# Optimization experiments

Hardware: AMD Instinct MI355X
Metric: run time of the kernel (lower is better)

## Reference

```python
import jax, jax.numpy as jnp
import numpy as np

N_NODES = 100000
N_EDGES = 1600000
NFEAT = 128
NHID = 128
NCLASS = 40


def gcn_conv(x, W, b, src, dst, n_nodes):
    """PyG-style GCNConv: x' = D^{-1/2}(A+I)D^{-1/2} (x W) + b."""
    h = x @ W  # [N, out]
    loop = jnp.arange(n_nodes, dtype=src.dtype)
    s = jnp.concatenate([src, loop])  # add self-loops
    d = jnp.concatenate([dst, loop])
    deg = jax.ops.segment_sum(jnp.ones_like(s, dtype=h.dtype), d, num_segments=n_nodes)
    dinv = jnp.where(deg > 0, jax.lax.rsqrt(deg), 0.0)
    norm = dinv[s] * dinv[d]  # [E+N]
    msg = h[s] * norm[:, None]  # gather + scale
    out = jax.ops.segment_sum(msg, d, num_segments=n_nodes)  # scatter-add
    return out + b


def setup_inputs() -> dict:
    key = jax.random.key(0)
    ks = jax.random.split(key, 6)
    x = jax.random.normal(ks[0], (N_NODES, NFEAT), dtype=jnp.float32)
    edge_index = jax.random.randint(ks[1], (2, N_EDGES), 0, N_NODES, dtype=jnp.int64)
    sc1 = 1.0 / np.sqrt(NFEAT)
    sc2 = 1.0 / np.sqrt(NHID)
    W1 = jax.random.normal(ks[2], (NFEAT, NHID), dtype=jnp.float32) * sc1
    b1 = jnp.zeros((NHID,), dtype=jnp.float32)
    Wm = jax.random.normal(ks[3], (NHID, NHID), dtype=jnp.float32) * sc2
    bm = jnp.zeros((NHID,), dtype=jnp.float32)
    W2 = jax.random.normal(ks[4], (NHID, NCLASS), dtype=jnp.float32) * sc2
    b2 = jnp.zeros((NCLASS,), dtype=jnp.float32)
    return {"x": x, "edge_index": edge_index, "W1": W1, "b1": b1,
            "Wm": Wm, "bm": bm, "W2": W2, "b2": b2}


def reference(x, edge_index, W1, b1, Wm, bm, W2, b2):
    # StandGCNX forward, eval mode (dropout = identity)
    src, dst = edge_index[0], edge_index[1]
    n = x.shape[0]
    h = jax.nn.relu(gcn_conv(x, W1, b1, src, dst, n))
    h = jax.nn.relu(gcn_conv(h, Wm, bm, src, dst, n))
    out = gcn_conv(h, W2, b2, src, dst, n)
    return out
```

## Files before the change

kernel.cpp:

```cpp
#include <hip/hip_runtime.h>
#include <hip/hip_bf16.h>

typedef __attribute__((ext_vector_type(8))) short bf16x8;
typedef __attribute__((ext_vector_type(4))) float f32x4;

__device__ __forceinline__ ushort bf16rne(float f) {
    uint u = __float_as_uint(f);
    return (ushort)((u + 0x7fffu + ((u >> 16) & 1u)) >> 16);
}
__device__ __forceinline__ void unpack2(uint p, float& a, float& b) {
    a = __uint_as_float(p << 16);
    b = __uint_as_float(p & 0xffff0000u);
}


__global__ __launch_bounds__(256) void k_pre1(const float* __restrict__ W1,
                                              const float* __restrict__ Wm,
                                              const float* __restrict__ W2,
                                              ushort* __restrict__ w1t,
                                              ushort* __restrict__ wmt,
                                              ushort* __restrict__ w2t,
                                              const int* __restrict__ dst,
                                              int* __restrict__ bcnt, int E) {
    __shared__ int hist[512];
    int b = blockIdx.x;
    int t = threadIdx.x;
    if (b < 152) {
        if (b < 64) {
            int i = b * 256 + t; int k = i >> 7, n = i & 127;
            w1t[n * 128 + k] = bf16rne(W1[k * 128 + n]);
        } else if (b < 128) {
            int i = (b - 64) * 256 + t; int k = i >> 7, n = i & 127;
            wmt[n * 128 + k] = bf16rne(Wm[k * 128 + n]);
        } else {
            int i = (b - 128) * 256 + t;
            if (i < 6144) {
                int n = i >> 7, k = i & 127;
                w2t[n * 128 + k] = (n < 40) ? bf16rne(W2[k * 40 + n]) : (ushort)0;
            }
        }
        return;
    }
    hist[t] = 0; hist[t + 256] = 0;
    __syncthreads();
    int off = (b - 152) * 4096;
    int cnt = min(4096, E - off);
    for (int i = t; i < cnt; i += 256) atomicAdd(&hist[dst[off + i] >> 8], 1);
    __syncthreads();
    if (hist[t]) atomicAdd(&bcnt[t], hist[t]);
    if (hist[t + 256]) atomicAdd(&bcnt[t + 256], hist[t + 256]);
}

__global__ void k_bscan(const int* __restrict__ bcnt, int* __restrict__ bbase,
                        int* __restrict__ bcur, int nbuck) {
    __shared__ int s[512];
    int t = threadIdx.x;
    s[t] = (t < nbuck) ? bcnt[t] : 0;
    __syncthreads();
    for (int d = 1; d < 512; d <<= 1) {
        int u = (t >= d) ? s[t - d] : 0;
        __syncthreads();
        if (t >= d) s[t] += u;
        __syncthreads();
    }
    int excl = (t == 0) ? 0 : s[t - 1];
    bbase[t] = excl;
    if (t < nbuck) bcur[t] = excl;
    if (t == 511) bbase[512] = s[511];
}

__global__ __launch_bounds__(256) void k_binpack(const int* __restrict__ src,
                                                 const int* __restrict__ dst,
                                                 int* __restrict__ bcur,
                                                 uint* __restrict__ pairbuf,
                                                 int E, int nbuck) {
    __shared__ int hist[512];
    __shared__ int scn[512];
    __shared__ int cur[512];
    __shared__ int gbase[512];
    __shared__ uint sorted[4096];
    int t = threadIdx.x;
    int off = blockIdx.x * 4096;
    int cnt = min(4096, E - off);

    hist[t] = 0; hist[t + 256] = 0;
    __syncthreads();
    for (int i = t; i < cnt; i += 256) {
        int b = dst[off + i] >> 8;
        atomicAdd(&hist[b], 1);
    }
    __syncthreads();
    scn[t] = hist[t]; scn[t + 256] = hist[t + 256];
    __syncthreads();
    for (int d = 1; d < 256; d <<= 1) {
        int u0 = (t >= d) ? scn[t - d] : 0;
        int u1 = (t >= d) ? scn[256 + t - d] : 0;
        __syncthreads();
        if (t >= d) { scn[t] += u0; scn[256 + t] += u1; }
        __syncthreads();
    }
    int tot0 = scn[255];
    scn[256 + t] += tot0;
    __syncthreads();
    cur[t] = (t == 0) ? 0 : scn[t - 1];
    cur[t + 256] = scn[t + 255];
    if (t < nbuck && hist[t] > 0) gbase[t] = atomicAdd(&bcur[t], hist[t]);
    int t2 = t + 256;
    if (t2 < nbuck && hist[t2] > 0) gbase[t2] = atomicAdd(&bcur[t2], hist[t2]);
    __syncthreads();
    for (int i = t; i < cnt; i += 256) {
        int d = dst[off + i];
        int s = src[off + i];
        int b = d >> 8;
        int pos = atomicAdd(&cur[b], 1);
        sorted[pos] = ((uint)(d & 255) << 24) | (uint)s;
    }
    __syncthreads();
    int wid = t >> 6, lane = t & 63;
    for (int b = wid; b < nbuck; b += 4) {
        int n = hist[b];
        if (n == 0) continue;
        int ls = (b == 0) ? 0 : scn[b - 1];
        int gb = gbase[b];
        for (int j = lane; j < n; j += 64)
            pairbuf[gb + j] = sorted[ls + j];
    }
}


#define CSR_CAP 5632
__global__ __launch_bounds__(256) void k_mega(const uint* __restrict__ pairbuf,
                                              const int* __restrict__ bbase,
                                              int* __restrict__ rowptr,
                                              float* __restrict__ dinv,
                                              int* __restrict__ csr,
                                              int N, int nbuck,
                                              const float* __restrict__ A,
                                              const ushort* __restrict__ Wt,
                                              ushort* __restrict__ C, int M) {
    __shared__ int lhist[256];
    __shared__ int scn[256];
    __shared__ int lcur[256];
    __shared__ int lcsr[CSR_CAP];
    int t = threadIdx.x;
    if ((int)blockIdx.x >= nbuck) {
        int blk = blockIdx.x - nbuck;
        int wave = t >> 6, lane = t & 63;
        int m16 = lane & 15, quad = lane >> 4;
        int rowA = blk * 64 + wave * 16 + m16;
        int rA = min(rowA, M - 1);
        const float4* A4 = (const float4*)A;

        f32x4 acc[8];
#pragma unroll
        for (int i = 0; i < 8; i++) acc[i] = (f32x4){0.f, 0.f, 0.f, 0.f};
#pragma unroll
        for (int it = 0; it < 4; it++) {
            float4 f0 = A4[(size_t)rA * 32 + 8 * it + 2 * quad];
            float4 f1 = A4[(size_t)rA * 32 + 8 * it + 2 * quad + 1];
            bf16x8 af;
            af[0] = (short)bf16rne(f0.x); af[1] = (short)bf16rne(f0.y);
            af[2] = (short)bf16rne(f0.z); af[3] = (short)bf16rne(f0.w);
            af[4] = (short)bf16rne(f1.x); af[5] = (short)bf16rne(f1.y);
            af[6] = (short)bf16rne(f1.z); af[7] = (short)bf16rne(f1.w);
#pragma unroll
            for (int nt = 0; nt < 8; nt++) {
                bf16x8 bfr = *(const bf16x8*)(Wt + (size_t)(nt * 16 + m16) * 128 + it * 32 + quad * 8);
                acc[nt] = __builtin_amdgcn_mfma_f32_16x16x32_bf16(af, bfr, acc[nt], 0, 0, 0);
            }
        }
        int rowBase = blk * 64 + wave * 16 + quad * 4;
#pragma unroll
        for (int nt = 0; nt < 8; nt++) {
            int col = nt * 16 + m16;
#pragma unroll
            for (int r = 0; r < 4; r++) {
                int row = rowBase + r;
                if (row < M) C[(size_t)row * 128 + col] = bf16rne(acc[nt][r]);
            }
        }
        return;
    }
    int b = blockIdx.x;
    int base = b << 8;
    int nn = min(256, N - base);
    int lo = bbase[b], hi = bbase[b + 1];
    int cnt = hi - lo;
    lhist[t] = 0;
    __syncthreads();
    for (int i = t; i < cnt; i += 256) atomicAdd(&lhist[pairbuf[lo + i] >> 24], 1);
    __syncthreads();
    int mydeg = lhist[t];
    scn[t] = mydeg;
    __syncthreads();
    for (int d = 1; d < 256; d <<= 1) {
        int u = (t >= d) ? scn[t - d] : 0;
        __syncthreads();
        if (t >= d) scn[t] += u;
        __syncthreads();
    }
    int excl = (t == 0) ? 0 : scn[t - 1];
    lcur[t] = excl;
    if (t < nn) {
        rowptr[base + t] = lo + excl;
        dinv[base + t] = rsqrtf((float)(mydeg + 1));
    }
    if (b == nbuck - 1 && t == 0) rowptr[N] = hi;
    __syncthreads();
    if (cnt <= CSR_CAP) {
        for (int i = t; i < cnt; i += 256) {
            uint p = pairbuf[lo + i];
            int pos = atomicAdd(&lcur[p >> 24], 1);
            lcsr[pos] = (int)(p & 0xFFFFFFu);
        }
        __syncthreads();
        for (int i = t; i < cnt; i += 256) csr[lo + i] = lcsr[i];
    } else {
        for (int i = t; i < cnt; i += 256) {
            uint p = pairbuf[lo + i];
            int pos = lo + atomicAdd(&lcur[p >> 24], 1);
            csr[pos] = (int)(p & 0xFFFFFFu);
        }
    }
}


template <int NT>
__device__ __forceinline__ void fused_agg_gemm(const ushort* __restrict__ g,
                                               const float* __restrict__ dinv,
                                               const int* __restrict__ rowptr,
                                               const int* __restrict__ csr,
                                               const float* __restrict__ bias,
                                               const ushort* __restrict__ Wt,
                                               ushort* __restrict__ C,
                                               int M, int ccols) {
    __shared__ ushort hs[32][136];
    __shared__ int nextNode;
    int t = threadIdx.x;
    if (t == 0) nextNode = 0;
    int l = t & 15;
    const uint4* g16 = (const uint4*)g;
    float4 bb0 = ((const float4*)bias)[2 * l];
    float4 bb1 = ((const float4*)bias)[2 * l + 1];
    __syncthreads();

    for (;;) {
        int idx = 0;
        if (l == 0) idx = atomicAdd(&nextNode, 1);
        idx = __shfl(idx, (t & 63) & ~15, 64);
        if (idx >= 32) break;
        int node = blockIdx.x * 32 + idx;
        int nd = min(node, M - 1);
        float dn = dinv[nd];
        float a[8];
        {
            uint4 p = g16[(size_t)nd * 16 + l];
            float u, v;
            unpack2(p.x, u, v); a[0] = u * dn; a[1] = v * dn;
            unpack2(p.y, u, v); a[2] = u * dn; a[3] = v * dn;
            unpack2(p.z, u, v); a[4] = u * dn; a[5] = v * dn;
            unpack2(p.w, u, v); a[6] = u * dn; a[7] = v * dn;
        }
        int e0 = rowptr[nd], e1 = rowptr[nd + 1];
        int e = e0;
        for (; e + 4 <= e1; e += 4) {
            int s0 = csr[e], s1 = csr[e + 1], s2 = csr[e + 2], s3 = csr[e + 3];
            float w0 = dinv[s0], w1 = dinv[s1], w2 = dinv[s2], w3 = dinv[s3];
            uint4 p0 = g16[(size_t)s0 * 16 + l];
            uint4 p1 = g16[(size_t)s1 * 16 + l];
            uint4 p2 = g16[(size_t)s2 * 16 + l];
            uint4 p3 = g16[(size_t)s3 * 16 + l];
            float u, v;
            unpack2(p0.x, u, v); a[0] += u * w0; a[1] += v * w0;
            unpack2(p0.y, u, v); a[2] += u * w0; a[3] += v * w0;
            unpack2(p0.z, u, v); a[4] += u * w0; a[5] += v * w0;
            unpack2(p0.w, u, v); a[6] += u * w0; a[7] += v * w0;
            unpack2(p1.x, u, v); a[0] += u * w1; a[1] += v * w1;
            unpack2(p1.y, u, v); a[2] += u * w1; a[3] += v * w1;
            unpack2(p1.z, u, v); a[4] += u * w1; a[5] += v * w1;
            unpack2(p1.w, u, v); a[6] += u * w1; a[7] += v * w1;
            unpack2(p2.x, u, v); a[0] += u * w2; a[1] += v * w2;
            unpack2(p2.y, u, v); a[2] += u * w2; a[3] += v * w2;
            unpack2(p2.z, u, v); a[4] += u * w2; a[5] += v * w2;
            unpack2(p2.w, u, v); a[6] += u * w2; a[7] += v * w2;
            unpack2(p3.x, u, v); a[0] += u * w3; a[1] += v * w3;
            unpack2(p3.y, u, v); a[2] += u * w3; a[3] += v * w3;
            unpack2(p3.z, u, v); a[4] += u * w3; a[5] += v * w3;
            unpack2(p3.w, u, v); a[6] += u * w3; a[7] += v * w3;
        }
        for (; e < e1; e++) {
            int s = csr[e];
            float w = dinv[s];
            uint4 p = g16[(size_t)s * 16 + l];
            float u, v;
            unpack2(p.x, u, v); a[0] += u * w; a[1] += v * w;
            unpack2(p.y, u, v); a[2] += u * w; a[3] += v * w;
            unpack2(p.z, u, v); a[4] += u * w; a[5] += v * w;
            unpack2(p.w, u, v); a[6] += u * w; a[7] += v * w;
        }
        float o0 = fmaxf(a[0] * dn + bb0.x, 0.f);
        float o1 = fmaxf(a[1] * dn + bb0.y, 0.f);
        float o2 = fmaxf(a[2] * dn + bb0.z, 0.f);
        float o3 = fmaxf(a[3] * dn + bb0.w, 0.f);
        float o4 = fmaxf(a[4] * dn + bb1.x, 0.f);
        float o5 = fmaxf(a[5] * dn + bb1.y, 0.f);
        float o6 = fmaxf(a[6] * dn + bb1.z, 0.f);
        float o7 = fmaxf(a[7] * dn + bb1.w, 0.f);
        uint4 qv;
        qv.x = (uint)bf16rne(o0) | ((uint)bf16rne(o1) << 16);
        qv.y = (uint)bf16rne(o2) | ((uint)bf16rne(o3) << 16);
        qv.z = (uint)bf16rne(o4) | ((uint)bf16rne(o5) << 16);
        qv.w = (uint)bf16rne(o6) | ((uint)bf16rne(o7) << 16);
        *(uint4*)&hs[idx][l * 8] = qv;
    }
    __syncthreads();

    int wave = t >> 6, lane = t & 63;
    int m16 = lane & 15, quad = lane >> 4;
    int rowHalf = wave & 1;
    int ntHalf = wave >> 1;
    constexpr int NTH = (NT + 1) / 2;
    int ntStart = ntHalf * NTH;
    int ntEnd = ntHalf ? NT : NTH;

    f32x4 acc[NTH];
#pragma unroll
    for (int i = 0; i < NTH; i++) acc[i] = (f32x4){0.f, 0.f, 0.f, 0.f};
#pragma unroll
    for (int it = 0; it < 4; it++) {
        bf16x8 af = *(const bf16x8*)&hs[rowHalf * 16 + m16][it * 32 + quad * 8];
        for (int nt = ntStart; nt < ntEnd; nt++) {
            bf16x8 bfr = *(const bf16x8*)(Wt + (size_t)(nt * 16 + m16) * 128 + it * 32 + quad * 8);
            acc[nt - ntStart] = __builtin_amdgcn_mfma_f32_16x16x32_bf16(af, bfr, acc[nt - ntStart], 0, 0, 0);
        }
    }
    int rowBase = blockIdx.x * 32 + rowHalf * 16 + quad * 4;
    for (int nt = ntStart; nt < ntEnd; nt++) {
        int col = nt * 16 + m16;
        if (col >= ccols) continue;
#pragma unroll
        for (int r = 0; r < 4; r++) {
            int row = rowBase + r;
            if (row < M) C[(size_t)row * ccols + col] = bf16rne(acc[nt - ntStart][r]);
        }
    }
}

__global__ __launch_bounds__(256) void k_fusedA(const ushort* __restrict__ g,
                                                const float* __restrict__ dinv,
                                                const int* __restrict__ rowptr,
                                                const int* __restrict__ csr,
                                                const float* __restrict__ bias,
                                                const ushort* __restrict__ Wt,
                                                ushort* __restrict__ C, int M) {
    fused_agg_gemm<8>(g, dinv, rowptr, csr, bias, Wt, C, M, 128);
}

__global__ __launch_bounds__(256) void k_fusedB(const ushort* __restrict__ g,
                                                const float* __restrict__ dinv,
                                                const int* __restrict__ rowptr,
                                                const int* __restrict__ csr,
                                                const float* __restrict__ bias,
                                                const ushort* __restrict__ Wt,
                                                ushort* __restrict__ C, int M) {
    fused_agg_gemm<3>(g, dinv, rowptr, csr, bias, Wt, C, M, 40);
}


__global__ __launch_bounds__(256) void k_agg40_b(const ushort* __restrict__ g3,
                                                 const float* __restrict__ dinv,
                                                 const int* __restrict__ rowptr,
                                                 const int* __restrict__ csr,
                                                 const float* __restrict__ bias,
                                                 float* __restrict__ out, int N) {
    int t = threadIdx.x;
    if (t >= 250) return;
    int grp = t / 10;
    int l = t - grp * 10;
    int node = blockIdx.x * 25 + grp;
    if (node >= N) return;
    const uint2* gp = (const uint2*)g3;
    float dn = dinv[node];
    float a0, a1, a2, a3;
    {
        uint2 p = gp[(size_t)node * 10 + l];
        float u, v;
        unpack2(p.x, u, v); a0 = u * dn; a1 = v * dn;
        unpack2(p.y, u, v); a2 = u * dn; a3 = v * dn;
    }
    int e0 = rowptr[node], e1 = rowptr[node + 1];
    int e = e0;
    for (; e + 4 <= e1; e += 4) {
        int s0 = csr[e], s1 = csr[e + 1], s2 = csr[e + 2], s3 = csr[e + 3];
        float w0 = dinv[s0], w1 = dinv[s1], w2 = dinv[s2], w3 = dinv[s3];
        uint2 p0 = gp[(size_t)s0 * 10 + l];
        uint2 p1 = gp[(size_t)s1 * 10 + l];
        uint2 p2 = gp[(size_t)s2 * 10 + l];
        uint2 p3 = gp[(size_t)s3 * 10 + l];
        float u, v;
        unpack2(p0.x, u, v); a0 += u * w0; a1 += v * w0;
        unpack2(p0.y, u, v); a2 += u * w0; a3 += v * w0;
        unpack2(p1.x, u, v); a0 += u * w1; a1 += v * w1;
        unpack2(p1.y, u, v); a2 += u * w1; a3 += v * w1;
        unpack2(p2.x, u, v); a0 += u * w2; a1 += v * w2;
        unpack2(p2.y, u, v); a2 += u * w2; a3 += v * w2;
        unpack2(p3.x, u, v); a0 += u * w3; a1 += v * w3;
        unpack2(p3.y, u, v); a2 += u * w3; a3 += v * w3;
    }
    for (; e < e1; e++) {
        int s = csr[e];
        float w = dinv[s];
        uint2 p = gp[(size_t)s * 10 + l];
        float u, v;
        unpack2(p.x, u, v); a0 += u * w; a1 += v * w;
        unpack2(p.y, u, v); a2 += u * w; a3 += v * w;
    }
    float4 bb = ((const float4*)bias)[l];
    float4 o;
    o.x = a0 * dn + bb.x;
    o.y = a1 * dn + bb.y;
    o.z = a2 * dn + bb.z;
    o.w = a3 * dn + bb.w;
    ((float4*)out)[(size_t)node * 10 + l] = o;
}


extern "C" void kernel_launch(void* const* d_in, const int* in_sizes, int n_in,
                              void* d_out, int out_size, void* d_ws, size_t ws_size,
                              hipStream_t stream) {
    const float* x  = (const float*)d_in[0];
    const int* eidx = (const int*)d_in[1];
    const float* W1 = (const float*)d_in[2];
    const float* b1 = (const float*)d_in[3];
    const float* Wm = (const float*)d_in[4];
    const float* bm = (const float*)d_in[5];
    const float* W2 = (const float*)d_in[6];
    const float* b2 = (const float*)d_in[7];
    float* out = (float*)d_out;

    int N = in_sizes[0] / 128;
    int E = in_sizes[1] / 2;
    const int* src = eidx;
    const int* dst = eidx + E;
    int nbuck = (N + 255) >> 8;
    int ntile = (E + 4095) / 4096;

    char* ws = (char*)d_ws;
    size_t off = 0;
    auto alloc = [&](size_t bytes) -> void* {
        void* p = ws + off;
        off += (bytes + 255) & ~(size_t)255;
        return p;
    };
    float*  dinv    = (float*)alloc((size_t)N * 4);
    int*    rowptr  = (int*)alloc(((size_t)N + 1) * 4);
    int*    csr     = (int*)alloc((size_t)E * 4);
    uint*   pairbuf = (uint*)alloc((size_t)E * 4);
    int*    bcnt    = (int*)alloc(512 * 4);
    int*    bbase   = (int*)alloc(513 * 4);
    int*    bcur    = (int*)alloc(512 * 4);
    ushort* w1t     = (ushort*)alloc(128 * 128 * 2);
    ushort* wmt     = (ushort*)alloc(128 * 128 * 2);
    ushort* w2t     = (ushort*)alloc(48 * 128 * 2);
    ushort* gbuf    = (ushort*)alloc((size_t)N * 128 * 2);
    ushort* gbuf2   = (ushort*)alloc((size_t)N * 128 * 2);
    ushort* g3      = (ushort*)alloc((size_t)N * 40 * 2);

    int gblk64 = (N + 63) / 64;
    int gblk32 = (N + 31) / 32;

    hipMemsetAsync(bcnt, 0, 512 * 4, stream);
    k_pre1<<<152 + ntile, 256, 0, stream>>>(W1, Wm, W2, w1t, wmt, w2t, dst, bcnt, E);
    k_bscan<<<1, 512, 0, stream>>>(bcnt, bbase, bcur, nbuck);
    k_binpack<<<ntile, 256, 0, stream>>>(src, dst, bcur, pairbuf, E, nbuck);
    k_mega<<<nbuck + gblk64, 256, 0, stream>>>(pairbuf, bbase, rowptr, dinv, csr,
                                               N, nbuck, x, w1t, gbuf, N);
    k_fusedA<<<gblk32, 256, 0, stream>>>(gbuf, dinv, rowptr, csr, b1, wmt, gbuf2, N);
    k_fusedB<<<gblk32, 256, 0, stream>>>(gbuf2, dinv, rowptr, csr, bm, w2t, g3, N);
    k_agg40_b<<<(N + 24) / 25, 256, 0, stream>>>(g3, dinv, rowptr, csr, b2, out, N);
}
```

Baseline: 391.0 us.

## Fold source-side dinv scaling into GEMM epilogue and move x@W1 into binpack kernel

The fused aggregation+GEMM kernels now multiply each output row by dinv before storing, so the next layer's neighbour aggregation can sum pre-scaled rows without a per-edge dinv gather and multiply. Layer 1 still gathers dinv per edge, while layers 2 and 3 drop those random loads. Separately, the first x@W1 GEMM now runs alongside the binpack kernel instead of the CSR-build kernel, and CSR build becomes its own launch. This cuts random per-edge memory traffic in two aggregations, at the cost of reshuffling which work runs concurrently.

```diff
diff --git a/kernel.cpp b/kernel.cpp
--- a/kernel.cpp
+++ b/kernel.cpp
@@ -69,20 +69,61 @@
     if (t == 511) bbase[512] = s[511];
 }
 
-__global__ __launch_bounds__(256) void k_binpack(const int* __restrict__ src,
-                                                 const int* __restrict__ dst,
-                                                 int* __restrict__ bcur,
-                                                 uint* __restrict__ pairbuf,
-                                                 int E, int nbuck) {
+
+__global__ __launch_bounds__(256) void k_pack_gemm(const int* __restrict__ src,
+                                                   const int* __restrict__ dst,
+                                                   int* __restrict__ bcur,
+                                                   uint* __restrict__ pairbuf,
+                                                   int E, int nbuck, int ntile,
+                                                   const float* __restrict__ A,
+                                                   const ushort* __restrict__ Wt,
+                                                   ushort* __restrict__ C, int M) {
     __shared__ int hist[512];
     __shared__ int scn[512];
     __shared__ int cur[512];
     __shared__ int gbase[512];
     __shared__ uint sorted[4096];
     int t = threadIdx.x;
+    if ((int)blockIdx.x >= ntile) {
+        int blk = blockIdx.x - ntile;
+        int wave = t >> 6, lane = t & 63;
+        int m16 = lane & 15, quad = lane >> 4;
+        int rowA = blk * 64 + wave * 16 + m16;
+        int rA = min(rowA, M - 1);
+        const float4* A4 = (const float4*)A;
+
+        f32x4 acc[8];
+#pragma unroll
+        for (int i = 0; i < 8; i++) acc[i] = (f32x4){0.f, 0.f, 0.f, 0.f};
+#pragma unroll
+        for (int it = 0; it < 4; it++) {
+            float4 f0 = A4[(size_t)rA * 32 + 8 * it + 2 * quad];
+            float4 f1 = A4[(size_t)rA * 32 + 8 * it + 2 * quad + 1];
+            bf16x8 af;
+            af[0] = (short)bf16rne(f0.x); af[1] = (short)bf16rne(f0.y);
+            af[2] = (short)bf16rne(f0.z); af[3] = (short)bf16rne(f0.w);
+            af[4] = (short)bf16rne(f1.x); af[5] = (short)bf16rne(f1.y);
+            af[6] = (short)bf16rne(f1.z); af[7] = (short)bf16rne(f1.w);
+#pragma unroll
+            for (int nt = 0; nt < 8; nt++) {
+                bf16x8 bfr = *(const bf16x8*)(Wt + (size_t)(nt * 16 + m16) * 128 + it * 32 + quad * 8);
+                acc[nt] = __builtin_amdgcn_mfma_f32_16x16x32_bf16(af, bfr, acc[nt], 0, 0, 0);
+            }
+        }
+        int rowBase = blk * 64 + wave * 16 + quad * 4;
+#pragma unroll
+        for (int nt = 0; nt < 8; nt++) {
+            int col = nt * 16 + m16;
+#pragma unroll
+            for (int r = 0; r < 4; r++) {
+                int row = rowBase + r;
+                if (row < M) C[(size_t)row * 128 + col] = bf16rne(acc[nt][r]);
+            }
+        }
+        return;
+    }
     int off = blockIdx.x * 4096;
     int cnt = min(4096, E - off);
-
     hist[t] = 0; hist[t + 256] = 0;
     __syncthreads();
     for (int i = t; i < cnt; i += 256) {
@@ -127,65 +168,23 @@
     }
 }
 
-
 #define CSR_CAP 5632
-__global__ __launch_bounds__(256) void k_mega(const uint* __restrict__ pairbuf,
-                                              const int* __restrict__ bbase,
-                                              int* __restrict__ rowptr,
-                                              float* __restrict__ dinv,
-                                              int* __restrict__ csr,
-                                              int N, int nbuck,
-                                              const float* __restrict__ A,
-                                              const ushort* __restrict__ Wt,
-                                              ushort* __restrict__ C, int M) {
+__global__ __launch_bounds__(256) void k_csrbuild(const uint* __restrict__ pairbuf,
+                                                  const int* __restrict__ bbase,
+                                                  int* __restrict__ rowptr,
+                                                  float* __restrict__ dinv,
+                                                  int* __restrict__ csr,
+                                                  int N, int nbuck) {
     __shared__ int lhist[256];
     __shared__ int scn[256];
     __shared__ int lcur[256];
     __shared__ int lcsr[CSR_CAP];
-    int t = threadIdx.x;
-    if ((int)blockIdx.x >= nbuck) {
-        int blk = blockIdx.x - nbuck;
-        int wave = t >> 6, lane = t & 63;
-        int m16 = lane & 15, quad = lane >> 4;
-        int rowA = blk * 64 + wave * 16 + m16;
-        int rA = min(rowA, M - 1);
-        const float4* A4 = (const float4*)A;
-
-        f32x4 acc[8];
-#pragma unroll
-        for (int i = 0; i < 8; i++) acc[i] = (f32x4){0.f, 0.f, 0.f, 0.f};
-#pragma unroll
-        for (int it = 0; it < 4; it++) {
-            float4 f0 = A4[(size_t)rA * 32 + 8 * it + 2 * quad];
-            float4 f1 = A4[(size_t)rA * 32 + 8 * it + 2 * quad + 1];
-            bf16x8 af;
-            af[0] = (short)bf16rne(f0.x); af[1] = (short)bf16rne(f0.y);
-            af[2] = (short)bf16rne(f0.z); af[3] = (short)bf16rne(f0.w);
-            af[4] = (short)bf16rne(f1.x); af[5] = (short)bf16rne(f1.y);
-            af[6] = (short)bf16rne(f1.z); af[7] = (short)bf16rne(f1.w);
-#pragma unroll
-            for (int nt = 0; nt < 8; nt++) {
-                bf16x8 bfr = *(const bf16x8*)(Wt + (size_t)(nt * 16 + m16) * 128 + it * 32 + quad * 8);
-                acc[nt] = __builtin_amdgcn_mfma_f32_16x16x32_bf16(af, bfr, acc[nt], 0, 0, 0);
-            }
-        }
-        int rowBase = blk * 64 + wave * 16 + quad * 4;
-#pragma unroll
-        for (int nt = 0; nt < 8; nt++) {
-            int col = nt * 16 + m16;
-#pragma unroll
-            for (int r = 0; r < 4; r++) {
-                int row = rowBase + r;
-                if (row < M) C[(size_t)row * 128 + col] = bf16rne(acc[nt][r]);
-            }
-        }
-        return;
-    }
     int b = blockIdx.x;
     int base = b << 8;
     int nn = min(256, N - base);
     int lo = bbase[b], hi = bbase[b + 1];
     int cnt = hi - lo;
+    int t = threadIdx.x;
     lhist[t] = 0;
     __syncthreads();
     for (int i = t; i < cnt; i += 256) atomicAdd(&lhist[pairbuf[lo + i] >> 24], 1);
@@ -225,7 +224,7 @@
 }
 
 
-template <int NT>
+template <int NT, bool EDGE_W>
 __device__ __forceinline__ void fused_agg_gemm(const ushort* __restrict__ g,
                                                const float* __restrict__ dinv,
                                                const int* __restrict__ rowptr,
@@ -256,41 +255,66 @@
         {
             uint4 p = g16[(size_t)nd * 16 + l];
             float u, v;
-            unpack2(p.x, u, v); a[0] = u * dn; a[1] = v * dn;
-            unpack2(p.y, u, v); a[2] = u * dn; a[3] = v * dn;
-            unpack2(p.z, u, v); a[4] = u * dn; a[5] = v * dn;
-            unpack2(p.w, u, v); a[6] = u * dn; a[7] = v * dn;
+            if (EDGE_W) {
+                unpack2(p.x, u, v); a[0] = u * dn; a[1] = v * dn;
+                unpack2(p.y, u, v); a[2] = u * dn; a[3] = v * dn;
+                unpack2(p.z, u, v); a[4] = u * dn; a[5] = v * dn;
+                unpack2(p.w, u, v); a[6] = u * dn; a[7] = v * dn;
+            } else {
+                unpack2(p.x, a[0], a[1]); unpack2(p.y, a[2], a[3]);
+                unpack2(p.z, a[4], a[5]); unpack2(p.w, a[6], a[7]);
+            }
         }
         int e0 = rowptr[nd], e1 = rowptr[nd + 1];
         int e = e0;
         for (; e + 4 <= e1; e += 4) {
             int s0 = csr[e], s1 = csr[e + 1], s2 = csr[e + 2], s3 = csr[e + 3];
-            float w0 = dinv[s0], w1 = dinv[s1], w2 = dinv[s2], w3 = dinv[s3];
+            float w0 = 1.f, w1 = 1.f, w2 = 1.f, w3 = 1.f;
+            if (EDGE_W) { w0 = dinv[s0]; w1 = dinv[s1]; w2 = dinv[s2]; w3 = dinv[s3]; }
             uint4 p0 = g16[(size_t)s0 * 16 + l];
             uint4 p1 = g16[(size_t)s1 * 16 + l];
             uint4 p2 = g16[(size_t)s2 * 16 + l];
             uint4 p3 = g16[(size_t)s3 * 16 + l];
             float u, v;
-            unpack2(p0.x, u, v); a[0] += u * w0; a[1] += v * w0;
-            unpack2(p0.y, u, v); a[2] += u * w0; a[3] += v * w0;
-            unpack2(p0.z, u, v); a[4] += u * w0; a[5] += v * w0;
-            unpack2(p0.w, u, v); a[6] += u * w0; a[7] += v * w0;
-            unpack2(p1.x, u, v); a[0] += u * w1; a[1] += v * w1;
-            unpack2(p1.y, u, v); a[2] += u * w1; a[3] += v * w1;
-            unpack2(p1.z, u, v); a[4] += u * w1; a[5] += v * w1;
-            unpack2(p1.w, u, v); a[6] += u * w1; a[7] += v * w1;
-            unpack2(p2.x, u, v); a[0] += u * w2; a[1] += v * w2;
-            unpack2(p2.y, u, v); a[2] += u * w2; a[3] += v * w2;
-            unpack2(p2.z, u, v); a[4] += u * w2; a[5] += v * w2;
-            unpack2(p2.w, u, v); a[6] += u * w2; a[7] += v * w2;
-            unpack2(p3.x, u, v); a[0] += u * w3; a[1] += v * w3;
-            unpack2(p3.y, u, v); a[2] += u * w3; a[3] += v * w3;
-            unpack2(p3.z, u, v); a[4] += u * w3; a[5] += v * w3;
-            unpack2(p3.w, u, v); a[6] += u * w3; a[7] += v * w3;
+            if (EDGE_W) {
+                unpack2(p0.x, u, v); a[0] += u * w0; a[1] += v * w0;
+                unpack2(p0.y, u, v); a[2] += u * w0; a[3] += v * w0;
+                unpack2(p0.z, u, v); a[4] += u * w0; a[5] += v * w0;
+                unpack2(p0.w, u, v); a[6] += u * w0; a[7] += v * w0;
+                unpack2(p1.x, u, v); a[0] += u * w1; a[1] += v * w1;
+                unpack2(p1.y, u, v); a[2] += u * w1; a[3] += v * w1;
+                unpack2(p1.z, u, v); a[4] += u * w1; a[5] += v * w1;
+                unpack2(p1.w, u, v); a[6] += u * w1; a[7] += v * w1;
+                unpack2(p2.x, u, v); a[0] += u * w2; a[1] += v * w2;
+                unpack2(p2.y, u, v); a[2] += u * w2; a[3] += v * w2;
+                unpack2(p2.z, u, v); a[4] += u * w2; a[5] += v * w2;
+                unpack2(p2.w, u, v); a[6] += u * w2; a[7] += v * w2;
+                unpack2(p3.x, u, v); a[0] += u * w3; a[1] += v * w3;
+                unpack2(p3.y, u, v); a[2] += u * w3; a[3] += v * w3;
+                unpack2(p3.z, u, v); a[4] += u * w3; a[5] += v * w3;
+                unpack2(p3.w, u, v); a[6] += u * w3; a[7] += v * w3;
+            } else {
+                unpack2(p0.x, u, v); a[0] += u; a[1] += v;
+                unpack2(p0.y, u, v); a[2] += u; a[3] += v;
+                unpack2(p0.z, u, v); a[4] += u; a[5] += v;
+                unpack2(p0.w, u, v); a[6] += u; a[7] += v;
+                unpack2(p1.x, u, v); a[0] += u; a[1] += v;
+                unpack2(p1.y, u, v); a[2] += u; a[3] += v;
+                unpack2(p1.z, u, v); a[4] += u; a[5] += v;
+                unpack2(p1.w, u, v); a[6] += u; a[7] += v;
+                unpack2(p2.x, u, v); a[0] += u; a[1] += v;
+                unpack2(p2.y, u, v); a[2] += u; a[3] += v;
+                unpack2(p2.z, u, v); a[4] += u; a[5] += v;
+                unpack2(p2.w, u, v); a[6] += u; a[7] += v;
+                unpack2(p3.x, u, v); a[0] += u; a[1] += v;
+                unpack2(p3.y, u, v); a[2] += u; a[3] += v;
+                unpack2(p3.z, u, v); a[4] += u; a[5] += v;
+                unpack2(p3.w, u, v); a[6] += u; a[7] += v;
+            }
         }
         for (; e < e1; e++) {
             int s = csr[e];
-            float w = dinv[s];
+            float w = EDGE_W ? dinv[s] : 1.f;
             uint4 p = g16[(size_t)s * 16 + l];
             float u, v;
             unpack2(p.x, u, v); a[0] += u * w; a[1] += v * w;
@@ -335,13 +359,16 @@
         }
     }
     int rowBase = blockIdx.x * 32 + rowHalf * 16 + quad * 4;
+    float dnv[4];
+#pragma unroll
+    for (int r = 0; r < 4; r++) dnv[r] = dinv[min(rowBase + r, M - 1)];
     for (int nt = ntStart; nt < ntEnd; nt++) {
         int col = nt * 16 + m16;
         if (col >= ccols) continue;
 #pragma unroll
         for (int r = 0; r < 4; r++) {
             int row = rowBase + r;
-            if (row < M) C[(size_t)row * ccols + col] = bf16rne(acc[nt - ntStart][r]);
+            if (row < M) C[(size_t)row * ccols + col] = bf16rne(acc[nt - ntStart][r] * dnv[r]);
         }
     }
 }
@@ -353,7 +380,7 @@
                                                 const float* __restrict__ bias,
                                                 const ushort* __restrict__ Wt,
                                                 ushort* __restrict__ C, int M) {
-    fused_agg_gemm<8>(g, dinv, rowptr, csr, bias, Wt, C, M, 128);
+    fused_agg_gemm<8, true>(g, dinv, rowptr, csr, bias, Wt, C, M, 128);
 }
 
 __global__ __launch_bounds__(256) void k_fusedB(const ushort* __restrict__ g,
@@ -363,7 +390,7 @@
                                                 const float* __restrict__ bias,
                                                 const ushort* __restrict__ Wt,
                                                 ushort* __restrict__ C, int M) {
-    fused_agg_gemm<3>(g, dinv, rowptr, csr, bias, Wt, C, M, 40);
+    fused_agg_gemm<3, false>(g, dinv, rowptr, csr, bias, Wt, C, M, 40);
 }
 
 
@@ -384,36 +411,33 @@
     float a0, a1, a2, a3;
     {
         uint2 p = gp[(size_t)node * 10 + l];
-        float u, v;
-        unpack2(p.x, u, v); a0 = u * dn; a1 = v * dn;
-        unpack2(p.y, u, v); a2 = u * dn; a3 = v * dn;
+        unpack2(p.x, a0, a1);
+        unpack2(p.y, a2, a3);
     }
     int e0 = rowptr[node], e1 = rowptr[node + 1];
     int e = e0;
     for (; e + 4 <= e1; e += 4) {
         int s0 = csr[e], s1 = csr[e + 1], s2 = csr[e + 2], s3 = csr[e + 3];
-        float w0 = dinv[s0], w1 = dinv[s1], w2 = dinv[s2], w3 = dinv[s3];
         uint2 p0 = gp[(size_t)s0 * 10 + l];
         uint2 p1 = gp[(size_t)s1 * 10 + l];
         uint2 p2 = gp[(size_t)s2 * 10 + l];
         uint2 p3 = gp[(size_t)s3 * 10 + l];
         float u, v;
-        unpack2(p0.x, u, v); a0 += u * w0; a1 += v * w0;
-        unpack2(p0.y, u, v); a2 += u * w0; a3 += v * w0;
-        unpack2(p1.x, u, v); a0 += u * w1; a1 += v * w1;
-        unpack2(p1.y, u, v); a2 += u * w1; a3 += v * w1;
-        unpack2(p2.x, u, v); a0 += u * w2; a1 += v * w2;
-        unpack2(p2.y, u, v); a2 += u * w2; a3 += v * w2;
-        unpack2(p3.x, u, v); a0 += u * w3; a1 += v * w3;
-        unpack2(p3.y, u, v); a2 += u * w3; a3 += v * w3;
+        unpack2(p0.x, u, v); a0 += u; a1 += v;
+        unpack2(p0.y, u, v); a2 += u; a3 += v;
+        unpack2(p1.x, u, v); a0 += u; a1 += v;
+        unpack2(p1.y, u, v); a2 += u; a3 += v;
+        unpack2(p2.x, u, v); a0 += u; a1 += v;
+        unpack2(p2.y, u, v); a2 += u; a3 += v;
+        unpack2(p3.x, u, v); a0 += u; a1 += v;
+        unpack2(p3.y, u, v); a2 += u; a3 += v;
     }
     for (; e < e1; e++) {
         int s = csr[e];
-        float w = dinv[s];
         uint2 p = gp[(size_t)s * 10 + l];
         float u, v;
-        unpack2(p.x, u, v); a0 += u * w; a1 += v * w;
-        unpack2(p.y, u, v); a2 += u * w; a3 += v * w;
+        unpack2(p.x, u, v); a0 += u; a1 += v;
+        unpack2(p.y, u, v); a2 += u; a3 += v;
     }
     float4 bb = ((const float4*)bias)[l];
     float4 o;
@@ -472,9 +496,9 @@
     hipMemsetAsync(bcnt, 0, 512 * 4, stream);
     k_pre1<<<152 + ntile, 256, 0, stream>>>(W1, Wm, W2, w1t, wmt, w2t, dst, bcnt, E);
     k_bscan<<<1, 512, 0, stream>>>(bcnt, bbase, bcur, nbuck);
-    k_binpack<<<ntile, 256, 0, stream>>>(src, dst, bcur, pairbuf, E, nbuck);
-    k_mega<<<nbuck + gblk64, 256, 0, stream>>>(pairbuf, bbase, rowptr, dinv, csr,
-                                               N, nbuck, x, w1t, gbuf, N);
+    k_pack_gemm<<<ntile + gblk64, 256, 0, stream>>>(src, dst, bcur, pairbuf, E, nbuck,
+                                                    ntile, x, w1t, gbuf, N);
+    k_csrbuild<<<nbuck, 256, 0, stream>>>(pairbuf, bbase, rowptr, dinv, csr, N, nbuck);
     k_fusedA<<<gblk32, 256, 0, stream>>>(gbuf, dinv, rowptr, csr, b1, wmt, gbuf2, N);
     k_fusedB<<<gblk32, 256, 0, stream>>>(gbuf2, dinv, rowptr, csr, bm, w2t, g3, N);
     k_agg40_b<<<(N + 24) / 25, 256, 0, stream>>>(g3, dinv, rowptr, csr, b2, out, N);
```

New measurement: 368.3 us. 1.06x faster.
